# Optimization experiments

Measured on AMD Instinct MI355X. Metric: run time of the kernel, lower is better.

The kernel has to match this reference:

```python
import jax, jax.numpy as jnp
import numpy as np

INPUT_SIZE = 2048
HIDDEN_SIZE = 2048
BATCH = 4096


def setup_inputs() -> dict:
    key = jax.random.key(0)
    ks = jax.random.split(key, 24)
    s_in = 1.0 / np.sqrt(INPUT_SIZE)
    s_h = 1.0 / np.sqrt(HIDDEN_SIZE)
    inp = {
        "x": jax.random.normal(ks[0], (BATCH, INPUT_SIZE), jnp.float32),
        "h_prev": jax.random.normal(ks[1], (BATCH, HIDDEN_SIZE), jnp.float32),
        "c_prev": jax.random.normal(ks[2], (BATCH, HIDDEN_SIZE), jnp.float32),
        "n_prev": jnp.ones((BATCH, HIDDEN_SIZE), jnp.float32),
        "m_prev": jnp.zeros((BATCH, HIDDEN_SIZE), jnp.float32),
    }
    # 4 input projections (W*x) and 4 recurrent projections (R*h), each Linear w/ bias.
    names_x = ["Wzx", "Wix", "Wfx", "Wox"]
    names_h = ["Rzh", "Rih", "Rfh", "Roh"]
    for j, n in enumerate(names_x):
        inp[n + "_w"] = jax.random.uniform(ks[3 + 2 * j], (HIDDEN_SIZE, INPUT_SIZE), jnp.float32, -s_in, s_in)
        inp[n + "_b"] = jax.random.uniform(ks[4 + 2 * j], (HIDDEN_SIZE,), jnp.float32, -s_in, s_in)
    for j, n in enumerate(names_h):
        inp[n + "_w"] = jax.random.uniform(ks[11 + 2 * j], (HIDDEN_SIZE, HIDDEN_SIZE), jnp.float32, -s_h, s_h)
        inp[n + "_b"] = jax.random.uniform(ks[12 + 2 * j], (HIDDEN_SIZE,), jnp.float32, -s_h, s_h)
    return inp


def _lin(x, w, b):
    return x @ w.T + b


def reference(x, h_prev, c_prev, n_prev, m_prev,
              Wzx_w, Wzx_b, Wix_w, Wix_b, Wfx_w, Wfx_b, Wox_w, Wox_b,
              Rzh_w, Rzh_b, Rih_w, Rih_b, Rfh_w, Rfh_b, Roh_w, Roh_b):
    z = jnp.tanh(_lin(x, Wzx_w, Wzx_b) + _lin(h_prev, Rzh_w, Rzh_b))
    # log(i) and log(f) are the pre-activations (i = exp(pre_i), f = exp(pre_f))
    log_i = _lin(x, Wix_w, Wix_b) + _lin(h_prev, Rih_w, Rih_b)
    log_f = _lin(x, Wfx_w, Wfx_b) + _lin(h_prev, Rfh_w, Rfh_b)
    o = jax.nn.sigmoid(_lin(x, Wox_w, Wox_b) + _lin(h_prev, Roh_w, Roh_b))
    m = jnp.maximum(log_f + m_prev, log_i)  # stabilizer state
    i_hat = jnp.exp(log_i - m)
    f_hat = jnp.exp(log_f + m_prev - m)
    c = f_hat * c_prev + i_hat * z
    n = f_hat * n_prev + i_hat
    h = o * c / n
    return (h, c, n, m)
```

## Files before the change

### kernel.cpp

```cpp
#include <hip/hip_runtime.h>
#include <hip/hip_bf16.h>


#define BATCH 4096
#define NHID  2048
#define KDIM  4096
#define NTOT  8388608L

typedef float  f32x4  __attribute__((ext_vector_type(4)));
typedef short  short8 __attribute__((ext_vector_type(8)));

#define GL_LDS16(gp, lp)                                                      \
    __builtin_amdgcn_global_load_lds(                                         \
        (const __attribute__((address_space(1))) void*)(gp),                  \
        (__attribute__((address_space(3))) void*)(lp), 16, 0, 0)

__device__ __forceinline__ unsigned short f2bf(float f) {
    unsigned u = __float_as_uint(f);
    unsigned r = (u + 0x7fffu + ((u >> 16) & 1u)) >> 16;
    return (unsigned short)r;
}

__global__ void convA_kernel(const float* __restrict__ x,
                             const float* __restrict__ h,
                             unsigned short* __restrict__ A) {
    int gid = blockIdx.x * 256 + threadIdx.x;
    int row = gid >> 10;
    int col = (gid & 1023) << 2;
    const float* src = (col < 2048) ? (x + (long)row * 2048 + col)
                                    : (h + (long)row * 2048 + (col - 2048));
    float4 v = *(const float4*)src;
    ushort4 o;
    o.x = f2bf(v.x); o.y = f2bf(v.y); o.z = f2bf(v.z); o.w = f2bf(v.w);
    *(ushort4*)(A + ((long)row << 12) + col) = o;
}

__global__ void convW_kernel(const float* __restrict__ w0, const float* __restrict__ w1,
                             const float* __restrict__ w2, const float* __restrict__ w3,
                             const float* __restrict__ w4, const float* __restrict__ w5,
                             const float* __restrict__ w6, const float* __restrict__ w7,
                             unsigned short* __restrict__ Wb) {
    int z = blockIdx.y;
    const float* src;
    switch (z) {
        case 0: src = w0; break; case 1: src = w1; break;
        case 2: src = w2; break; case 3: src = w3; break;
        case 4: src = w4; break; case 5: src = w5; break;
        case 6: src = w6; break; default: src = w7; break;
    }
    int gid = blockIdx.x * 256 + threadIdx.x;
    int row = gid >> 9;
    int col = (gid & 511) << 2;
    float4 v = *(const float4*)(src + (long)row * 2048 + col);
    ushort4 o;
    o.x = f2bf(v.x); o.y = f2bf(v.y); o.z = f2bf(v.z); o.w = f2bf(v.w);
    int g = z & 3, hf = z >> 2;
    *(ushort4*)(Wb + (long)g * NHID * KDIM + (long)row * KDIM + hf * 2048 + col) = o;
}

__global__ void bias_kernel(const float* __restrict__ b0, const float* __restrict__ b1,
                            const float* __restrict__ b2, const float* __restrict__ b3,
                            const float* __restrict__ r0, const float* __restrict__ r1,
                            const float* __restrict__ r2, const float* __restrict__ r3,
                            float* __restrict__ Bb) {
    int gid = blockIdx.x * 256 + threadIdx.x;
    int g = gid >> 11, j = gid & 2047;
    const float *wb, *rb;
    switch (g) {
        case 0: wb = b0; rb = r0; break; case 1: wb = b1; rb = r1; break;
        case 2: wb = b2; rb = r2; break; default: wb = b3; rb = r3; break;
    }
    Bb[gid] = wb[j] + rb[j];
}

__global__ __launch_bounds__(256, 3) void slstm_kernel(
    const __hip_bfloat16* __restrict__ A,
    const __hip_bfloat16* __restrict__ W,
    const float* __restrict__ Bb,
    const float* __restrict__ c_prev,
    const float* __restrict__ n_prev,
    const float* __restrict__ m_prev,
    float* __restrict__ out)
{
    __shared__ uint4 smem4[40960 / 16];
    char* smem = (char*)smem4;

    const int tid  = threadIdx.x;
    const int lane = tid & 63;
    const int wv   = tid >> 6;
    const int lm   = lane & 15;
    const int quad = lane >> 4;
    const int l7   = lm & 7;

    const int row0 = blockIdx.x * 64;
    const int col0 = blockIdx.y * 64;

    int gofsA[2]; char* ldsA[2];
#pragma unroll
    for (int t = 0; t < 2; ++t) {
        int idx = (wv * 2 + t) * 64 + lane;
        int r = idx >> 3, jj = idx & 7;
        int j = jj ^ (r & 7);
        gofsA[t] = (row0 + r) * KDIM + j * 8;
        ldsA[t]  = smem + (wv * 2 + t) * 1024;
    }
    int gofsB[8]; char* ldsB[8];
#pragma unroll
    for (int t = 0; t < 8; ++t) {
        int idx = (wv * 8 + t) * 64 + lane;
        int g = idx >> 9, rr = (idx >> 3) & 63, jj = idx & 7;
        int j = jj ^ (rr & 7);
        gofsB[t] = (g * NHID + col0 + rr) * KDIM + j * 8;
        ldsB[t]  = smem + 8192 + (wv * 8 + t) * 1024;
    }

    f32x4 acc[4][4];
#pragma unroll
    for (int mt = 0; mt < 4; ++mt)
#pragma unroll
        for (int nt = 0; nt < 4; ++nt)
#pragma unroll
            for (int r = 0; r < 4; ++r) acc[mt][nt][r] = 0.0f;

    for (int kt = 0; kt < KDIM / 64; ++kt) {
        const int k0 = kt * 64;
        __syncthreads();
#pragma unroll
        for (int t = 0; t < 2; ++t) GL_LDS16(A + gofsA[t] + k0, ldsA[t]);
#pragma unroll
        for (int t = 0; t < 8; ++t) GL_LDS16(W + gofsB[t] + k0, ldsB[t]);
        __syncthreads();
#pragma unroll
        for (int kk = 0; kk < 2; ++kk) {
            const int cof = ((kk * 4 + quad) ^ l7) * 16;
            short8 af[4], bf[4];
#pragma unroll
            for (int mt = 0; mt < 4; ++mt)
                af[mt] = *(const short8*)(smem + (mt * 16 + lm) * 128 + cof);
#pragma unroll
            for (int nt = 0; nt < 4; ++nt)
                bf[nt] = *(const short8*)(smem + 8192 + wv * 8192 + (nt * 16 + lm) * 128 + cof);
#pragma unroll
            for (int mt = 0; mt < 4; ++mt)
#pragma unroll
                for (int nt = 0; nt < 4; ++nt)
                    acc[mt][nt] = __builtin_amdgcn_mfma_f32_16x16x32_bf16(
                        af[mt], bf[nt], acc[mt][nt], 0, 0, 0);
        }
    }

    float* exch = (float*)smem;
#pragma unroll
    for (int mt = 0; mt < 4; ++mt) {
        __syncthreads();
#pragma unroll
        for (int nt = 0; nt < 4; ++nt)
#pragma unroll
            for (int r = 0; r < 4; ++r)
                exch[(wv * 16 + quad * 4 + r) * 65 + nt * 16 + lm] = acc[mt][nt][r];
        __syncthreads();
#pragma unroll
        for (int q = 0; q < 4; ++q) {
            int e   = q * 256 + tid;
            int row = e >> 6, col = e & 63;
            int R = row0 + mt * 16 + row;
            int C = col0 + col;
            long idx = (long)R * NHID + C;
            float zp = exch[(0 * 16 + row) * 65 + col] + Bb[C];
            float ip = exch[(1 * 16 + row) * 65 + col] + Bb[2048 + C];
            float fp = exch[(2 * 16 + row) * 65 + col] + Bb[4096 + C];
            float op = exch[(3 * 16 + row) * 65 + col] + Bb[6144 + C];
            float cp = c_prev[idx], np = n_prev[idx], mp = m_prev[idx];
            float z  = tanhf(zp);
            float o  = 1.0f / (1.0f + __expf(-op));
            float mm = fmaxf(fp + mp, ip);
            float ih = __expf(ip - mm);
            float fh = __expf(fp + mp - mm);
            float cc = fh * cp + ih * z;
            float nn = fh * np + ih;
            float hh = o * cc / nn;
            out[idx]            = hh;
            out[NTOT + idx]     = cc;
            out[2 * NTOT + idx] = nn;
            out[3 * NTOT + idx] = mm;
        }
    }
}

extern "C" void kernel_launch(void* const* d_in, const int* in_sizes, int n_in,
                              void* d_out, int out_size, void* d_ws, size_t ws_size,
                              hipStream_t stream) {
    const float* x      = (const float*)d_in[0];
    const float* h_prev = (const float*)d_in[1];
    const float* c_prev = (const float*)d_in[2];
    const float* n_prev = (const float*)d_in[3];
    const float* m_prev = (const float*)d_in[4];
    unsigned short* A  = (unsigned short*)d_ws;
    unsigned short* Wb = (unsigned short*)((char*)d_ws + 33554432);
    float*          Bb = (float*)((char*)d_ws + 100663296);

    convA_kernel<<<16384, 256, 0, stream>>>(x, h_prev, A);
    convW_kernel<<<dim3(4096, 8), 256, 0, stream>>>(
        (const float*)d_in[5], (const float*)d_in[7], (const float*)d_in[9],
        (const float*)d_in[11], (const float*)d_in[13], (const float*)d_in[15],
        (const float*)d_in[17], (const float*)d_in[19], Wb);
    bias_kernel<<<32, 256, 0, stream>>>(
        (const float*)d_in[6], (const float*)d_in[8], (const float*)d_in[10],
        (const float*)d_in[12], (const float*)d_in[14], (const float*)d_in[16],
        (const float*)d_in[18], (const float*)d_in[20], Bb);

    slstm_kernel<<<dim3(64, 32), 256, 0, stream>>>(
        (const __hip_bfloat16*)A, (const __hip_bfloat16*)Wb, Bb,
        c_prev, n_prev, m_prev, (float*)d_out);
}
```

Before: 660.6 us.

## Double GEMM block rows with 512-thread blocks; widen conversion kernels; add nontemporal I/O

The main GEMM block now covers 128 rows instead of 64 and runs 8 waves, each wave owning one gate and one row half, so every weight tile loaded into LDS is reused by twice as many rows. This cuts weight traffic per output and halves the grid. The conversion kernels now process 8 elements per thread, and the epilogue and conversions use nontemporal loads and stores to avoid polluting the cache. The cost is more LDS per block (48 KB) and a launch bound of 512 threads with 4 blocks per CU, which adds register pressure and may lower occupancy.

```diff
diff --git a/kernel.cpp b/kernel.cpp
--- a/kernel.cpp
+++ b/kernel.cpp
@@ -6,9 +6,11 @@
 #define NHID  2048
 #define KDIM  4096
 #define NTOT  8388608L
-
-typedef float  f32x4  __attribute__((ext_vector_type(4)));
-typedef short  short8 __attribute__((ext_vector_type(8)));
+#define AW_OFS 16777216
+
+typedef float  f32x4   __attribute__((ext_vector_type(4)));
+typedef short  short8  __attribute__((ext_vector_type(8)));
+typedef unsigned short ushort8 __attribute__((ext_vector_type(8)));
 
 #define GL_LDS16(gp, lp)                                                      \
     __builtin_amdgcn_global_load_lds(                                         \
@@ -25,14 +27,16 @@
                              const float* __restrict__ h,
                              unsigned short* __restrict__ A) {
     int gid = blockIdx.x * 256 + threadIdx.x;
-    int row = gid >> 10;
-    int col = (gid & 1023) << 2;
+    int row = gid >> 9;
+    int col = (gid & 511) << 3;
     const float* src = (col < 2048) ? (x + (long)row * 2048 + col)
                                     : (h + (long)row * 2048 + (col - 2048));
-    float4 v = *(const float4*)src;
-    ushort4 o;
-    o.x = f2bf(v.x); o.y = f2bf(v.y); o.z = f2bf(v.z); o.w = f2bf(v.w);
-    *(ushort4*)(A + ((long)row << 12) + col) = o;
+    f32x4 v0 = __builtin_nontemporal_load((const f32x4*)src);
+    f32x4 v1 = __builtin_nontemporal_load((const f32x4*)src + 1);
+    ushort8 o;
+    o[0] = f2bf(v0[0]); o[1] = f2bf(v0[1]); o[2] = f2bf(v0[2]); o[3] = f2bf(v0[3]);
+    o[4] = f2bf(v1[0]); o[5] = f2bf(v1[1]); o[6] = f2bf(v1[2]); o[7] = f2bf(v1[3]);
+    *(ushort8*)(A + ((long)row << 12) + col) = o;
 }
 
 __global__ void convW_kernel(const float* __restrict__ w0, const float* __restrict__ w1,
@@ -49,13 +53,16 @@
         case 6: src = w6; break; default: src = w7; break;
     }
     int gid = blockIdx.x * 256 + threadIdx.x;
-    int row = gid >> 9;
-    int col = (gid & 511) << 2;
-    float4 v = *(const float4*)(src + (long)row * 2048 + col);
-    ushort4 o;
-    o.x = f2bf(v.x); o.y = f2bf(v.y); o.z = f2bf(v.z); o.w = f2bf(v.w);
+    int row = gid >> 8;
+    int col = (gid & 255) << 3;
+    const float* p = src + (long)row * 2048 + col;
+    f32x4 v0 = __builtin_nontemporal_load((const f32x4*)p);
+    f32x4 v1 = __builtin_nontemporal_load((const f32x4*)p + 1);
+    ushort8 o;
+    o[0] = f2bf(v0[0]); o[1] = f2bf(v0[1]); o[2] = f2bf(v0[2]); o[3] = f2bf(v0[3]);
+    o[4] = f2bf(v1[0]); o[5] = f2bf(v1[1]); o[6] = f2bf(v1[2]); o[7] = f2bf(v1[3]);
     int g = z & 3, hf = z >> 2;
-    *(ushort4*)(Wb + (long)g * NHID * KDIM + (long)row * KDIM + hf * 2048 + col) = o;
+    *(ushort8*)(Wb + (long)g * NHID * KDIM + (long)row * KDIM + hf * 2048 + col) = o;
 }
 
 __global__ void bias_kernel(const float* __restrict__ b0, const float* __restrict__ b1,
@@ -73,45 +80,46 @@
     Bb[gid] = wb[j] + rb[j];
 }
 
-__global__ __launch_bounds__(256, 3) void slstm_kernel(
+__global__ __launch_bounds__(512, 4) void slstm_kernel(
     const __hip_bfloat16* __restrict__ A,
-    const __hip_bfloat16* __restrict__ W,
     const float* __restrict__ Bb,
     const float* __restrict__ c_prev,
     const float* __restrict__ n_prev,
     const float* __restrict__ m_prev,
     float* __restrict__ out)
 {
-    __shared__ uint4 smem4[40960 / 16];
+    __shared__ uint4 smem4[49152 / 16];
     char* smem = (char*)smem4;
 
     const int tid  = threadIdx.x;
     const int lane = tid & 63;
     const int wv   = tid >> 6;
+    const int gate = wv & 3;
+    const int rh   = wv >> 2;
     const int lm   = lane & 15;
     const int quad = lane >> 4;
     const int l7   = lm & 7;
 
-    const int row0 = blockIdx.x * 64;
+    const int row0 = blockIdx.x * 128;
     const int col0 = blockIdx.y * 64;
 
-    int gofsA[2]; char* ldsA[2];
-#pragma unroll
-    for (int t = 0; t < 2; ++t) {
-        int idx = (wv * 2 + t) * 64 + lane;
-        int r = idx >> 3, jj = idx & 7;
-        int j = jj ^ (r & 7);
-        gofsA[t] = (row0 + r) * KDIM + j * 8;
-        ldsA[t]  = smem + (wv * 2 + t) * 1024;
-    }
-    int gofsB[8]; char* ldsB[8];
-#pragma unroll
-    for (int t = 0; t < 8; ++t) {
-        int idx = (wv * 8 + t) * 64 + lane;
-        int g = idx >> 9, rr = (idx >> 3) & 63, jj = idx & 7;
-        int j = jj ^ (rr & 7);
-        gofsB[t] = (g * NHID + col0 + rr) * KDIM + j * 8;
-        ldsB[t]  = smem + 8192 + (wv * 8 + t) * 1024;
+    int gofs[6]; char* lds[6];
+#pragma unroll
+    for (int t = 0; t < 6; ++t) {
+        int id = wv * 6 + t;
+        if (id < 16) {
+            int idx = id * 64 + lane;
+            int r = idx >> 3, jj = idx & 7;
+            int j = jj ^ (r & 7);
+            gofs[t] = (row0 + r) * KDIM + j * 8;
+            lds[t]  = smem + id * 1024;
+        } else {
+            int idx = (id - 16) * 64 + lane;
+            int g = idx >> 9, rr = (idx >> 3) & 63, jj = idx & 7;
+            int j = jj ^ (rr & 7);
+            gofs[t] = AW_OFS + (g * NHID + col0 + rr) * KDIM + j * 8;
+            lds[t]  = smem + 16384 + (id - 16) * 1024;
+        }
     }
 
     f32x4 acc[4][4];
@@ -121,14 +129,15 @@
         for (int nt = 0; nt < 4; ++nt)
 #pragma unroll
             for (int r = 0; r < 4; ++r) acc[mt][nt][r] = 0.0f;
+
+    const char* aB = smem + rh * 8192;
+    const char* bB = smem + 16384 + gate * 8192;
 
     for (int kt = 0; kt < KDIM / 64; ++kt) {
         const int k0 = kt * 64;
         __syncthreads();
 #pragma unroll
-        for (int t = 0; t < 2; ++t) GL_LDS16(A + gofsA[t] + k0, ldsA[t]);
-#pragma unroll
-        for (int t = 0; t < 8; ++t) GL_LDS16(W + gofsB[t] + k0, ldsB[t]);
+        for (int t = 0; t < 6; ++t) GL_LDS16(A + gofs[t] + k0, lds[t]);
         __syncthreads();
 #pragma unroll
         for (int kk = 0; kk < 2; ++kk) {
@@ -136,10 +145,10 @@
             short8 af[4], bf[4];
 #pragma unroll
             for (int mt = 0; mt < 4; ++mt)
-                af[mt] = *(const short8*)(smem + (mt * 16 + lm) * 128 + cof);
+                af[mt] = *(const short8*)(aB + (mt * 16 + lm) * 128 + cof);
 #pragma unroll
             for (int nt = 0; nt < 4; ++nt)
-                bf[nt] = *(const short8*)(smem + 8192 + wv * 8192 + (nt * 16 + lm) * 128 + cof);
+                bf[nt] = *(const short8*)(bB + (nt * 16 + lm) * 128 + cof);
 #pragma unroll
             for (int mt = 0; mt < 4; ++mt)
 #pragma unroll
@@ -157,20 +166,23 @@
         for (int nt = 0; nt < 4; ++nt)
 #pragma unroll
             for (int r = 0; r < 4; ++r)
-                exch[(wv * 16 + quad * 4 + r) * 65 + nt * 16 + lm] = acc[mt][nt][r];
+                exch[((rh * 4 + gate) * 16 + quad * 4 + r) * 65 + nt * 16 + lm] =
+                    acc[mt][nt][r];
         __syncthreads();
 #pragma unroll
         for (int q = 0; q < 4; ++q) {
-            int e   = q * 256 + tid;
-            int row = e >> 6, col = e & 63;
-            int R = row0 + mt * 16 + row;
+            int e   = q * 512 + tid;
+            int erh = e >> 10, row = (e >> 6) & 15, col = e & 63;
+            int R = row0 + erh * 64 + mt * 16 + row;
             int C = col0 + col;
             long idx = (long)R * NHID + C;
-            float zp = exch[(0 * 16 + row) * 65 + col] + Bb[C];
-            float ip = exch[(1 * 16 + row) * 65 + col] + Bb[2048 + C];
-            float fp = exch[(2 * 16 + row) * 65 + col] + Bb[4096 + C];
-            float op = exch[(3 * 16 + row) * 65 + col] + Bb[6144 + C];
-            float cp = c_prev[idx], np = n_prev[idx], mp = m_prev[idx];
+            float zp = exch[((erh * 4 + 0) * 16 + row) * 65 + col] + Bb[C];
+            float ip = exch[((erh * 4 + 1) * 16 + row) * 65 + col] + Bb[2048 + C];
+            float fp = exch[((erh * 4 + 2) * 16 + row) * 65 + col] + Bb[4096 + C];
+            float op = exch[((erh * 4 + 3) * 16 + row) * 65 + col] + Bb[6144 + C];
+            float cp = __builtin_nontemporal_load(c_prev + idx);
+            float np = __builtin_nontemporal_load(n_prev + idx);
+            float mp = __builtin_nontemporal_load(m_prev + idx);
             float z  = tanhf(zp);
             float o  = 1.0f / (1.0f + __expf(-op));
             float mm = fmaxf(fp + mp, ip);
@@ -179,10 +191,10 @@
             float cc = fh * cp + ih * z;
             float nn = fh * np + ih;
             float hh = o * cc / nn;
-            out[idx]            = hh;
-            out[NTOT + idx]     = cc;
-            out[2 * NTOT + idx] = nn;
-            out[3 * NTOT + idx] = mm;
+            __builtin_nontemporal_store(hh, out + idx);
+            __builtin_nontemporal_store(cc, out + NTOT + idx);
+            __builtin_nontemporal_store(nn, out + 2 * NTOT + idx);
+            __builtin_nontemporal_store(mm, out + 3 * NTOT + idx);
         }
     }
 }
@@ -199,8 +211,8 @@
     unsigned short* Wb = (unsigned short*)((char*)d_ws + 33554432);
     float*          Bb = (float*)((char*)d_ws + 100663296);
 
-    convA_kernel<<<16384, 256, 0, stream>>>(x, h_prev, A);
-    convW_kernel<<<dim3(4096, 8), 256, 0, stream>>>(
+    convA_kernel<<<8192, 256, 0, stream>>>(x, h_prev, A);
+    convW_kernel<<<dim3(2048, 8), 256, 0, stream>>>(
         (const float*)d_in[5], (const float*)d_in[7], (const float*)d_in[9],
         (const float*)d_in[11], (const float*)d_in[13], (const float*)d_in[15],
         (const float*)d_in[17], (const float*)d_in[19], Wb);
@@ -209,7 +221,6 @@
         (const float*)d_in[12], (const float*)d_in[14], (const float*)d_in[16],
         (const float*)d_in[18], (const float*)d_in[20], Bb);
 
-    slstm_kernel<<<dim3(64, 32), 256, 0, stream>>>(
-        (const __hip_bfloat16*)A, (const __hip_bfloat16*)Wb, Bb,
-        c_prev, n_prev, m_prev, (float*)d_out);
-}
+    slstm_kernel<<<dim3(32, 32), 512, 0, stream>>>(
+        (const __hip_bfloat16*)A, Bb, c_prev, n_prev, m_prev, (float*)d_out);
+}
```

New measurement: 582.0 us. 11.9% less time.
